# Optimization experiments

Hardware: AMD Instinct MI355X
Metric: run time of the kernel (lower is better)

Reference implementation:

```python
import jax, jax.numpy as jnp
import numpy as np

V, D, L = 256, 512, 12
B, S = 8, 8192
EPS = 1e-5


def layernorm(x, g, b):
    mu = jnp.mean(x, axis=-1, keepdims=True)
    var = jnp.var(x, axis=-1, keepdims=True)
    return (x - mu) * jax.lax.rsqrt(var + EPS) * g + b


def log_g(x):
    # log of g(x) = x+0.5 if x>=0 else sigmoid(x)
    return jnp.where(x >= 0, jnp.log(jax.nn.relu(x) + 0.5), -jax.nn.softplus(-x))


def heinsen_scan_log(log_coeffs, log_values):
    # h_t = a_t * h_{t-1} + b_t in log-space, parallel over seq (axis=1)
    a_star = jnp.cumsum(log_coeffs, axis=1)
    log_h0_plus_b = jax.lax.cumlogsumexp(log_values - a_star, axis=1)
    return jnp.exp(a_star + log_h0_plus_b)


def min_gru(x, W):
    hg = x @ W                      # [B,S,2D]
    hidden, gate = hg[..., :D], hg[..., D:]
    log_coeffs = -jax.nn.softplus(gate)      # log(1 - z)
    log_z = -jax.nn.softplus(-gate)          # log z
    log_values = log_z + log_g(hidden)
    return heinsen_scan_log(log_coeffs, log_values)


def setup_inputs() -> dict:
    key = jax.random.key(0)
    k0, k1, k2 = jax.random.split(key, 3)
    tokens = jax.random.randint(k0, (B, S), 0, V)
    emb = jax.random.normal(k1, (V, D), dtype=jnp.float32) * 0.02
    # xavier uniform for Linear(D, 2D): fan_in=D, fan_out=2D
    lim = float(np.sqrt(6.0 / (D + 2 * D)))
    W = jax.random.uniform(k2, (L, D, 2 * D), minval=-lim, maxval=lim, dtype=jnp.float32)
    return {
        "tokens": tokens,
        "emb": emb,
        "ln_g": jnp.ones((L, D), jnp.float32),
        "ln_b": jnp.zeros((L, D), jnp.float32),
        "W": W,
        "norm_g": jnp.ones((D,), jnp.float32),
        "norm_b": jnp.zeros((D,), jnp.float32),
    }


def reference(tokens, emb, ln_g, ln_b, W, norm_g, norm_b):
    x = emb[tokens]                 # [B,S,D]
    for i in range(L):
        h = layernorm(x, ln_g[i], ln_b[i])
        x = x + min_gru(h, W[i])
    x = layernorm(x, norm_g, norm_b)
    logits = x @ emb.T              # tied lm_head, [B,S,V]
    return logits
```

## Files before the change

### kernel.cpp

```cpp
#include <hip/hip_runtime.h>
#include <stdint.h>

#define D 512
#define VOCAB 256
#define NLAYER 12
#define BB 8
#define SS 8192
#define CH 128
#define SL 64

typedef __bf16 bf16x8 __attribute__((ext_vector_type(8)));
typedef float f32x4 __attribute__((ext_vector_type(4)));
typedef _Float16 half2_t __attribute__((ext_vector_type(2)));

__device__ __forceinline__ unsigned short f2bf(float f) {
  union { float f; uint32_t u; } c; c.f = f;
  uint32_t u = c.u;
  u += 0x7FFFu + ((u >> 16) & 1u);
  return (unsigned short)(u >> 16);
}

__device__ __forceinline__ float rcpf_(float x) { return __builtin_amdgcn_rcpf(x); }

__device__ __forceinline__ uint32_t pack_fv(float f, float v) {
  union { half2_t h; uint32_t u; } c;
  c.h.x = (_Float16)f;
  c.h.y = (_Float16)v;
  return c.u;
}

__device__ __forceinline__ void unpack_fv(uint32_t u, float& f, float& v) {
  union { uint32_t u; half2_t h; } c; c.u = u;
  f = (float)c.h.x;
  v = (float)c.h.y;
}

__device__ __forceinline__ void gl_lds16(const unsigned short* g, unsigned short* l) {
  __builtin_amdgcn_global_load_lds((const __attribute__((address_space(1))) void*)(const void*)g,
                                   (__attribute__((address_space(3))) void*)(void*)l, 16, 0, 0);
}

__global__ __launch_bounds__(256) void k_gather(const int* __restrict__ toks,
                                                const float* __restrict__ emb,
                                                const float* __restrict__ g,
                                                const float* __restrict__ b,
                                                float* __restrict__ x,
                                                unsigned short* __restrict__ o) {
  int T = blockIdx.x * 256 + threadIdx.x;
  int row = T >> 6, lane = T & 63;
  int tok = toks[row] & (VOCAB - 1);
  const float4* s = (const float4*)(emb + (size_t)tok * D) + lane * 2;
  float4 v0 = s[0], v1 = s[1];
  float4* d = (float4*)(x + (size_t)row * D) + lane * 2;
  d[0] = v0;
  d[1] = v1;
  float sm = v0.x + v0.y + v0.z + v0.w + v1.x + v1.y + v1.z + v1.w;
  float ss = v0.x * v0.x + v0.y * v0.y + v0.z * v0.z + v0.w * v0.w +
             v1.x * v1.x + v1.y * v1.y + v1.z * v1.z + v1.w * v1.w;
  for (int m = 32; m; m >>= 1) {
    sm += __shfl_xor(sm, m, 64);
    ss += __shfl_xor(ss, m, 64);
  }
  float mu = sm * (1.0f / 512.0f);
  float var = ss * (1.0f / 512.0f) - mu * mu;
  float rstd = rsqrtf(var + 1e-5f);
  const float4* gp = (const float4*)g + lane * 2;
  const float4* bp = (const float4*)b + lane * 2;
  float4 g0 = gp[0], g1 = gp[1], b0 = bp[0], b1 = bp[1];
  uint32_t w0 = (uint32_t)f2bf((v0.x - mu) * rstd * g0.x + b0.x) |
                ((uint32_t)f2bf((v0.y - mu) * rstd * g0.y + b0.y) << 16);
  uint32_t w1 = (uint32_t)f2bf((v0.z - mu) * rstd * g0.z + b0.z) |
                ((uint32_t)f2bf((v0.w - mu) * rstd * g0.w + b0.w) << 16);
  uint32_t w2 = (uint32_t)f2bf((v1.x - mu) * rstd * g1.x + b1.x) |
                ((uint32_t)f2bf((v1.y - mu) * rstd * g1.y + b1.y) << 16);
  uint32_t w3 = (uint32_t)f2bf((v1.z - mu) * rstd * g1.z + b1.z) |
                ((uint32_t)f2bf((v1.w - mu) * rstd * g1.w + b1.w) << 16);
  uint4 r; r.x = w0; r.y = w1; r.z = w2; r.w = w3;
  ((uint4*)(o + (size_t)row * D))[lane] = r;
}

__global__ __launch_bounds__(256) void k_convW(const float* __restrict__ W,
                                               unsigned short* __restrict__ Wt) {
  __shared__ float tile[32][33];
  int bid = blockIdx.x;
  int l = bid >> 9;
  int rem = bid & 511;
  int kt = rem >> 5, nt = rem & 31;
  int k0 = kt * 32, n0 = nt * 32;
  int tx = threadIdx.x & 31, ty = threadIdx.x >> 5;
  const float* Wl = W + (size_t)l * D * 2 * D;
  for (int i = 0; i < 4; i++) {
    int k = k0 + ty + 8 * i;
    tile[ty + 8 * i][tx] = Wl[(size_t)k * 1024 + n0 + tx];
  }
  __syncthreads();
  unsigned short* Wtl = Wt + (size_t)l * 1024 * D;
  for (int i = 0; i < 4; i++) {
    int n = n0 + ty + 8 * i;
    Wtl[(size_t)n * D + k0 + tx] = f2bf(tile[tx][ty + 8 * i]);
  }
}

__global__ __launch_bounds__(256) void k_fragW(const unsigned short* __restrict__ Wt,
                                               unsigned short* __restrict__ WtF) {
  int t = blockIdx.x * 256 + threadIdx.x;
  int lane = t & 63;
  int tile = t >> 6;
  int l = tile >> 10;
  int rem = tile & 1023;
  int n16 = rem >> 4, kt = rem & 15;
  const unsigned short* src = Wt + (size_t)l * 1024 * 512 +
                              (size_t)(n16 * 16 + (lane & 15)) * 512 + kt * 32 + (lane >> 4) * 8;
  *(uint4*)(WtF + (size_t)l * 524288 + ((size_t)rem * 64 + lane) * 8) = *(const uint4*)src;
}

__global__ __launch_bounds__(256) void k_convEmb(const float* __restrict__ e,
                                                 unsigned short* __restrict__ o) {
  int t = blockIdx.x * 256 + threadIdx.x;
  const float4* s = (const float4*)e + (size_t)t * 2;
  float4 a = s[0], b = s[1];
  uint32_t w0 = (uint32_t)f2bf(a.x) | ((uint32_t)f2bf(a.y) << 16);
  uint32_t w1 = (uint32_t)f2bf(a.z) | ((uint32_t)f2bf(a.w) << 16);
  uint32_t w2 = (uint32_t)f2bf(b.x) | ((uint32_t)f2bf(b.y) << 16);
  uint32_t w3 = (uint32_t)f2bf(b.z) | ((uint32_t)f2bf(b.w) << 16);
  uint4 r; r.x = w0; r.y = w1; r.z = w2; r.w = w3;
  ((uint4*)o)[t] = r;
}

__global__ __launch_bounds__(256, 2) void k_gemm_act(const unsigned short* __restrict__ A,
                                                     const unsigned short* __restrict__ Bt,
                                                     uint32_t* __restrict__ fv,
                                                     float* __restrict__ P,
                                                     float* __restrict__ Q) {
  __shared__ __align__(16) unsigned short As[64 * 512];
  const int tid = threadIdx.x;
  const int lane = tid & 63;
  const int wave = tid >> 6;
  const int m0 = blockIdx.x * 64;
  const int qm = lane & 15;
  const int hi = lane >> 4;
  for (int j = 0; j < 16; j++) {
    int r = wave * 16 + j;
    int cg = (lane & ~7) | ((lane & 7) ^ (r & 7));
    gl_lds16(A + (size_t)(m0 + r) * 512 + cg * 8, As + r * 512);
  }
  __syncthreads();

  const int b_loc = m0 >> 13;
  const int c_chunk = (m0 & (SS - 1)) >> 6;
  const size_t pq0 = ((size_t)b_loc * CH + c_chunk) * 512;

  for (int np = 0; np < 2; np++) {
    const int c0 = np * 256 + wave * 64;
    const int n16h = (c0 >> 4);
    f32x4 ah[4][4] = {};
    f32x4 ag[4][4] = {};
    bf16x8 bh[2][4], bg[2][4];
    for (int j = 0; j < 4; j++) {
      bh[0][j] = *(const bf16x8*)(Bt + (((size_t)(n16h + j) * 16 + 0) * 64 + lane) * 8);
      bg[0][j] = *(const bf16x8*)(Bt + (((size_t)(n16h + j + 32) * 16 + 0) * 64 + lane) * 8);
    }
    for (int kt = 0; kt < 16; kt++) {
      const int cur = kt & 1;
      if (kt < 15) {
        const int nxt = cur ^ 1;
        for (int j = 0; j < 4; j++) {
          bh[nxt][j] = *(const bf16x8*)(Bt + (((size_t)(n16h + j) * 16 + kt + 1) * 64 + lane) * 8);
          bg[nxt][j] = *(const bf16x8*)(Bt + (((size_t)(n16h + j + 32) * 16 + kt + 1) * 64 + lane) * 8);
        }
      }
      bf16x8 af[4];
      for (int i = 0; i < 4; i++) {
        int row = i * 16 + qm;
        int cgd = kt * 4 + hi;
        int cl = (cgd & ~7) | ((cgd & 7) ^ (row & 7));
        af[i] = *(const bf16x8*)(&As[row * 512 + cl * 8]);
      }
      for (int i = 0; i < 4; i++)
        for (int j = 0; j < 4; j++) {
          ah[i][j] = __builtin_amdgcn_mfma_f32_16x16x32_bf16(af[i], bh[cur][j], ah[i][j], 0, 0, 0);
          ag[i][j] = __builtin_amdgcn_mfma_f32_16x16x32_bf16(af[i], bg[cur][j], ag[i][j], 0, 0, 0);
        }
    }
    const int rq = hi * 4;
    for (int j = 0; j < 4; j++) {
      float cp = 1.f, cq = 0.f;
      for (int i = 0; i < 4; i++) {
        float sp = 1.f, sq = 0.f;
        for (int r = 0; r < 4; r++) {
          float h = ah[i][j][r];
          float g = ag[i][j][r];
          float e = __expf(g);
          float f = rcpf_(1.0f + e);
          float sg = 1.0f - f;
          float gf = h >= 0.0f ? h + 0.5f : rcpf_(1.0f + __expf(-h));
          float v = sg * gf;
          int rowg = m0 + i * 16 + rq + r;
          fv[(size_t)rowg * 512 + c0 + j * 16 + qm] = pack_fv(f, v);
          sp *= f;
          sq = sq * f + v;
        }
        float op = __shfl_xor(sp, 16), oq = __shfl_xor(sq, 16);
        float tp = sp * op;
        float tq = (lane & 16) ? (oq * sp + sq) : (sq * op + oq);
        op = __shfl_xor(tp, 32); oq = __shfl_xor(tq, 32);
        sp = tp * op;
        sq = (lane & 32) ? (oq * tp + tq) : (tq * op + oq);
        cq = cq * sp + sq;
        cp = cp * sp;
      }
      if (hi == 0) {
        P[pq0 + c0 + j * 16 + qm] = cp;
        Q[pq0 + c0 + j * 16 + qm] = cq;
      }
    }
  }
}

__global__ __launch_bounds__(256) void k_gemm(const unsigned short* __restrict__ A,
                                              const unsigned short* __restrict__ Bt,
                                              float* __restrict__ C, int N, int MT) {
  __shared__ __align__(16) unsigned short As[128 * 64];
  __shared__ __align__(16) unsigned short Bs[128 * 64];
  const int tid = threadIdx.x;
  const int lane = tid & 63;
  const int wave = tid >> 6;
  const int bid = blockIdx.x;
  const int mt = bid % MT;
  const int nt = bid / MT;
  const int m0 = mt * 128, n0 = nt * 128;
  const int wr = (wave >> 1) * 64;
  const int wc = (wave & 1) * 64;
  const int lrow = lane >> 3;
  const int lcs = ((lane & 7) ^ lrow) * 8;
  const unsigned short* Ag = A + (size_t)(m0 + wave * 32 + lrow) * 512 + lcs;
  const unsigned short* Bg = Bt + (size_t)(n0 + wave * 32 + lrow) * 512 + lcs;
  unsigned short* Al = As + wave * 32 * 64;
  unsigned short* Bl = Bs + wave * 32 * 64;
  const int qm = lane & 15;
  const int hi = lane >> 4;
  f32x4 acc[4][4] = {};
  for (int k0 = 0; k0 < 512; k0 += 64) {
    for (int j = 0; j < 4; j++) gl_lds16(Ag + k0 + (size_t)j * 8 * 512, Al + j * 512);
    for (int j = 0; j < 4; j++) gl_lds16(Bg + k0 + (size_t)j * 8 * 512, Bl + j * 512);
    __syncthreads();
    for (int ks = 0; ks < 2; ks++) {
      const int sw = ((ks * 4 + hi) ^ (qm & 7)) * 8;
      bf16x8 af[4], bfr[4];
      for (int i = 0; i < 4; i++) {
        af[i] = *(const bf16x8*)(&As[(wr + i * 16 + qm) * 64 + sw]);
        bfr[i] = *(const bf16x8*)(&Bs[(wc + i * 16 + qm) * 64 + sw]);
      }
      for (int i = 0; i < 4; i++)
        for (int j = 0; j < 4; j++)
          acc[i][j] = __builtin_amdgcn_mfma_f32_16x16x32_bf16(af[i], bfr[j], acc[i][j], 0, 0, 0);
    }
    __syncthreads();
  }
  const int col = lane & 15;
  const int rq = (lane >> 4) * 4;
  for (int i = 0; i < 4; i++)
    for (int j = 0; j < 4; j++)
      for (int r = 0; r < 4; r++)
        C[(size_t)(m0 + wr + i * 16 + rq + r) * N + (n0 + wc + j * 16 + col)] = acc[i][j][r];
}

__global__ __launch_bounds__(512) void k_scan2(const float* __restrict__ P,
                                               const float* __restrict__ Q,
                                               float* __restrict__ Hs) {
  __shared__ float lp[8][64];
  __shared__ float lq[8][64];
  const int lane = threadIdx.x & 63;
  const int w = threadIdx.x >> 6;
  const int dg = blockIdx.x & 7;
  const int b = blockIdx.x >> 3;
  const int d = dg * 64 + lane;
  const int c0 = w * 16;
  const size_t base = (size_t)b * CH * 512 + d;
  float p = 1.f, q = 0.f;
  for (int c = c0; c < c0 + 16; c++) {
    size_t i = base + (size_t)c * 512;
    float Pc = P[i], Qc = Q[i];
    q = q * Pc + Qc;
    p = p * Pc;
  }
  lp[w][lane] = p;
  lq[w][lane] = q;
  __syncthreads();
  float qq = 0.f, pp = 1.f;
  for (int ww = 0; ww < w; ww++) {
    float a = lp[ww][lane], bq = lq[ww][lane];
    qq = qq * a + bq;
    pp = pp * a;
  }
  float h = qq;
  for (int c = c0; c < c0 + 16; c++) {
    size_t i = base + (size_t)c * 512;
    Hs[i] = h;
    h = P[i] * h + Q[i];
  }
  (void)pp;
}

__global__ __launch_bounds__(512) void k_scan3(const uint32_t* __restrict__ fv,
                                               const float* __restrict__ Hs,
                                               float* __restrict__ x,
                                               const float* __restrict__ g,
                                               const float* __restrict__ b,
                                               unsigned short* __restrict__ o) {
  const int d = threadIdx.x;
  const int bc = blockIdx.x;
  const int c = bc & (CH - 1);
  const int bb = bc >> 7;
  const size_t row0 = ((size_t)bb * SS + (size_t)c * SL);
  const uint32_t* base = fv + row0 * 512 + d;
  float* xb = x + row0 * 512 + d;
  float h = Hs[(size_t)bc * 512 + d];
  for (int s = 0; s < SL; s++) {
    float f, v;
    unpack_fv(base[(size_t)s * 512], f, v);
    h = f * h + v;
    xb[(size_t)s * 512] += h;
  }
  __syncthreads();

  const int wv = threadIdx.x >> 6, lane = threadIdx.x & 63;
  const float4* gp = (const float4*)g + lane * 2;
  const float4* bp = (const float4*)b + lane * 2;
  float4 g0 = gp[0], g1 = gp[1], b0 = bp[0], b1 = bp[1];
  const float* xr0 = x + row0 * 512;
  for (int rr = 0; rr < 8; rr++) {
    int r = wv * 8 + rr;
    const float4* xr = (const float4*)(xr0 + (size_t)r * 512) + lane * 2;
    float4 v0 = xr[0], v1 = xr[1];
    float sm = v0.x + v0.y + v0.z + v0.w + v1.x + v1.y + v1.z + v1.w;
    float ss = v0.x * v0.x + v0.y * v0.y + v0.z * v0.z + v0.w * v0.w +
               v1.x * v1.x + v1.y * v1.y + v1.z * v1.z + v1.w * v1.w;
    for (int m = 32; m; m >>= 1) {
      sm += __shfl_xor(sm, m, 64);
      ss += __shfl_xor(ss, m, 64);
    }
    float mu = sm * (1.0f / 512.0f);
    float var = ss * (1.0f / 512.0f) - mu * mu;
    float rstd = rsqrtf(var + 1e-5f);
    uint32_t w0 = (uint32_t)f2bf((v0.x - mu) * rstd * g0.x + b0.x) |
                  ((uint32_t)f2bf((v0.y - mu) * rstd * g0.y + b0.y) << 16);
    uint32_t w1 = (uint32_t)f2bf((v0.z - mu) * rstd * g0.z + b0.z) |
                  ((uint32_t)f2bf((v0.w - mu) * rstd * g0.w + b0.w) << 16);
    uint32_t w2 = (uint32_t)f2bf((v1.x - mu) * rstd * g1.x + b1.x) |
                  ((uint32_t)f2bf((v1.y - mu) * rstd * g1.y + b1.y) << 16);
    uint32_t w3 = (uint32_t)f2bf((v1.z - mu) * rstd * g1.z + b1.z) |
                  ((uint32_t)f2bf((v1.w - mu) * rstd * g1.w + b1.w) << 16);
    uint4 rr4; rr4.x = w0; rr4.y = w1; rr4.z = w2; rr4.w = w3;
    ((uint4*)(o + (row0 + r) * 512))[lane] = rr4;
  }
}

extern "C" void kernel_launch(void* const* d_in, const int* in_sizes, int n_in,
                              void* d_out, int out_size, void* d_ws, size_t ws_size,
                              hipStream_t stream) {
  const int* toks = (const int*)d_in[0];
  const float* emb = (const float*)d_in[1];
  const float* ln_g = (const float*)d_in[2];
  const float* ln_b = (const float*)d_in[3];
  const float* W = (const float*)d_in[4];
  const float* norm_g = (const float*)d_in[5];
  const float* norm_b = (const float*)d_in[6];
  float* out = (float*)d_out;

  const int gbs[4] = {8, 4, 2, 1};
  int GB = 1;
  for (int i = 0; i < 4; i++) {
    size_t MGv = (size_t)gbs[i] * SS;
    size_t need = MGv * 5120 + 2 * 12582912 + 262144 + (size_t)gbs[i] * 786432;
    if (need <= ws_size) { GB = gbs[i]; break; }
  }
  const int MG = GB * SS;
  const int MT128 = MG / 128;

  char* p = (char*)d_ws;
  float* x = (float*)p;                     p += (size_t)MG * 2048;
  uint32_t* fv = (uint32_t*)p;              p += (size_t)MG * 2048;
  unsigned short* hbf = (unsigned short*)p; p += (size_t)MG * 1024;
  unsigned short* Wtrow = (unsigned short*)p; p += 12582912;
  unsigned short* WtF = (unsigned short*)p;   p += 12582912;
  unsigned short* ebf = (unsigned short*)p;   p += 262144;
  float* P = (float*)p;                     p += (size_t)GB * 262144;
  float* Q = (float*)p;                     p += (size_t)GB * 262144;
  float* Hs = (float*)p;

  k_convW<<<NLAYER * 512, 256, 0, stream>>>(W, Wtrow);
  k_fragW<<<NLAYER * 1024 * 64 / 256, 256, 0, stream>>>(Wtrow, WtF);
  k_convEmb<<<64, 256, 0, stream>>>(emb, ebf);

  for (int g = 0; g < BB / GB; g++) {
    const int* tg = toks + (size_t)g * MG;
    float* outg = out + (size_t)g * MG * VOCAB;

    k_gather<<<MG / 4, 256, 0, stream>>>(tg, emb, ln_g, ln_b, x, hbf);
    for (int l = 0; l < NLAYER; l++) {
      k_gemm_act<<<MG / 64, 256, 0, stream>>>(hbf, WtF + (size_t)l * 524288, fv, P, Q);
      k_scan2<<<GB * 8, 512, 0, stream>>>(P, Q, Hs);
      const float* gn = (l < NLAYER - 1) ? (ln_g + (size_t)(l + 1) * D) : norm_g;
      const float* bn = (l < NLAYER - 1) ? (ln_b + (size_t)(l + 1) * D) : norm_b;
      k_scan3<<<GB * CH, 512, 0, stream>>>(fv, Hs, x, gn, bn, hbf);
    }
    k_gemm<<<2 * MT128, 256, 0, stream>>>(hbf, ebf, outg, VOCAB, MT128);
  }
}
```

Measured before the change: 2.894 ms.

## Fuse scan apply and layernorm into next layer's GEMM via chunk-local prefix scan

The GEMM epilogue now computes an intra-chunk inclusive prefix (cumulative F and local y) per row, so the final hidden state is just y + F*h0 with no sequential dependency. Applying that correction, the residual add and the next layer's layernorm are folded into the prologue of the following layer's GEMM kernel, which removes the separate per-layer scan3 launch and its sequential 64-step loop. Only one apply+LN kernel remains after the last layer. In exchange the GEMM kernel does extra global reads and writes of x and yF before its LDS load, waits on a full vmcnt drain, and the epilogue shuffle work grows.

```diff
diff --git a/kernel.cpp b/kernel.cpp
--- a/kernel.cpp
+++ b/kernel.cpp
@@ -127,11 +127,16 @@
   ((uint4*)o)[t] = r;
 }
 
-__global__ __launch_bounds__(256, 2) void k_gemm_act(const unsigned short* __restrict__ A,
+__global__ __launch_bounds__(256, 2) void k_gemm_act(float* __restrict__ X,
+                                                     uint32_t* __restrict__ yF,
+                                                     const float* __restrict__ Hs,
+                                                     const float* __restrict__ lng,
+                                                     const float* __restrict__ lnb,
+                                                     unsigned short* __restrict__ Ah,
                                                      const unsigned short* __restrict__ Bt,
-                                                     uint32_t* __restrict__ fv,
                                                      float* __restrict__ P,
-                                                     float* __restrict__ Q) {
+                                                     float* __restrict__ Q,
+                                                     int APPLY) {
   __shared__ __align__(16) unsigned short As[64 * 512];
   const int tid = threadIdx.x;
   const int lane = tid & 63;
@@ -139,16 +144,63 @@
   const int m0 = blockIdx.x * 64;
   const int qm = lane & 15;
   const int hi = lane >> 4;
+  const int b_loc = m0 >> 13;
+  const int c_chunk = (m0 & (SS - 1)) >> 6;
+  const size_t pq0 = ((size_t)b_loc * CH + c_chunk) * 512;
+
+  if (APPLY) {
+    const float4* hp = (const float4*)(Hs + pq0) + lane * 2;
+    float4 h0v = hp[0], h1v = hp[1];
+    const float4* gp = (const float4*)lng + lane * 2;
+    const float4* bp = (const float4*)lnb + lane * 2;
+    float4 gg0 = gp[0], gg1 = gp[1], bb0 = bp[0], bb1 = bp[1];
+    for (int j = 0; j < 16; j++) {
+      size_t row = (size_t)(m0 + wave * 16 + j);
+      float4* xp = (float4*)(X + row * 512) + lane * 2;
+      float4 x0 = xp[0], x1 = xp[1];
+      const uint4* yp = (const uint4*)(yF + row * 512) + lane * 2;
+      uint4 y0 = yp[0], y1 = yp[1];
+      float Ff, yy;
+      unpack_fv(y0.x, Ff, yy); x0.x += yy + Ff * h0v.x;
+      unpack_fv(y0.y, Ff, yy); x0.y += yy + Ff * h0v.y;
+      unpack_fv(y0.z, Ff, yy); x0.z += yy + Ff * h0v.z;
+      unpack_fv(y0.w, Ff, yy); x0.w += yy + Ff * h0v.w;
+      unpack_fv(y1.x, Ff, yy); x1.x += yy + Ff * h1v.x;
+      unpack_fv(y1.y, Ff, yy); x1.y += yy + Ff * h1v.y;
+      unpack_fv(y1.z, Ff, yy); x1.z += yy + Ff * h1v.z;
+      unpack_fv(y1.w, Ff, yy); x1.w += yy + Ff * h1v.w;
+      xp[0] = x0; xp[1] = x1;
+      float sm = x0.x + x0.y + x0.z + x0.w + x1.x + x1.y + x1.z + x1.w;
+      float ss = x0.x * x0.x + x0.y * x0.y + x0.z * x0.z + x0.w * x0.w +
+                 x1.x * x1.x + x1.y * x1.y + x1.z * x1.z + x1.w * x1.w;
+      for (int m = 32; m; m >>= 1) {
+        sm += __shfl_xor(sm, m, 64);
+        ss += __shfl_xor(ss, m, 64);
+      }
+      float mu = sm * (1.0f / 512.0f);
+      float var = ss * (1.0f / 512.0f) - mu * mu;
+      float rstd = rsqrtf(var + 1e-5f);
+      uint32_t w0 = (uint32_t)f2bf((x0.x - mu) * rstd * gg0.x + bb0.x) |
+                    ((uint32_t)f2bf((x0.y - mu) * rstd * gg0.y + bb0.y) << 16);
+      uint32_t w1 = (uint32_t)f2bf((x0.z - mu) * rstd * gg0.z + bb0.z) |
+                    ((uint32_t)f2bf((x0.w - mu) * rstd * gg0.w + bb0.w) << 16);
+      uint32_t w2 = (uint32_t)f2bf((x1.x - mu) * rstd * gg1.x + bb1.x) |
+                    ((uint32_t)f2bf((x1.y - mu) * rstd * gg1.y + bb1.y) << 16);
+      uint32_t w3 = (uint32_t)f2bf((x1.z - mu) * rstd * gg1.z + bb1.z) |
+                    ((uint32_t)f2bf((x1.w - mu) * rstd * gg1.w + bb1.w) << 16);
+      uint4 rr; rr.x = w0; rr.y = w1; rr.z = w2; rr.w = w3;
+      ((uint4*)(Ah + row * 512))[lane] = rr;
+    }
+    asm volatile("s_waitcnt vmcnt(0)" ::: "memory");
+    __builtin_amdgcn_sched_barrier(0);
+  }
+
   for (int j = 0; j < 16; j++) {
     int r = wave * 16 + j;
     int cg = (lane & ~7) | ((lane & 7) ^ (r & 7));
-    gl_lds16(A + (size_t)(m0 + r) * 512 + cg * 8, As + r * 512);
+    gl_lds16(Ah + (size_t)(m0 + r) * 512 + cg * 8, As + r * 512);
   }
   __syncthreads();
-
-  const int b_loc = m0 >> 13;
-  const int c_chunk = (m0 & (SS - 1)) >> 6;
-  const size_t pq0 = ((size_t)b_loc * CH + c_chunk) * 512;
 
   for (int np = 0; np < 2; np++) {
     const int c0 = np * 256 + wave * 64;
@@ -184,9 +236,11 @@
     }
     const int rq = hi * 4;
     for (int j = 0; j < 4; j++) {
-      float cp = 1.f, cq = 0.f;
+      float Bp = 1.f, Bq = 0.f;
       for (int i = 0; i < 4; i++) {
+        float fr[4], vr[4];
         float sp = 1.f, sq = 0.f;
+#pragma unroll
         for (int r = 0; r < 4; r++) {
           float h = ah[i][j][r];
           float g = ag[i][j][r];
@@ -195,23 +249,33 @@
           float sg = 1.0f - f;
           float gf = h >= 0.0f ? h + 0.5f : rcpf_(1.0f + __expf(-h));
           float v = sg * gf;
+          fr[r] = f; vr[r] = v;
+          sq = sq * f + v;
+          sp *= f;
+        }
+        float Ip = sp, Iq = sq;
+        float tp = __shfl_up(Ip, 16, 64), tq = __shfl_up(Iq, 16, 64);
+        if (hi >= 1) { Iq = tq * Ip + Iq; Ip = tp * Ip; }
+        tp = __shfl_up(Ip, 32, 64); tq = __shfl_up(Iq, 32, 64);
+        if (hi >= 2) { Iq = tq * Ip + Iq; Ip = tp * Ip; }
+        float Ep = __shfl_up(Ip, 16, 64), Eq = __shfl_up(Iq, 16, 64);
+        if (hi == 0) { Ep = 1.f; Eq = 0.f; }
+        float Tp = __shfl(Ip, 48 + qm, 64), Tq = __shfl(Iq, 48 + qm, 64);
+        float yv = Bq * Ep + Eq;
+        float Fv = Bp * Ep;
+#pragma unroll
+        for (int r = 0; r < 4; r++) {
+          yv = fr[r] * yv + vr[r];
+          Fv = Fv * fr[r];
           int rowg = m0 + i * 16 + rq + r;
-          fv[(size_t)rowg * 512 + c0 + j * 16 + qm] = pack_fv(f, v);
-          sp *= f;
-          sq = sq * f + v;
+          yF[(size_t)rowg * 512 + c0 + j * 16 + qm] = pack_fv(Fv, yv);
         }
-        float op = __shfl_xor(sp, 16), oq = __shfl_xor(sq, 16);
-        float tp = sp * op;
-        float tq = (lane & 16) ? (oq * sp + sq) : (sq * op + oq);
-        op = __shfl_xor(tp, 32); oq = __shfl_xor(tq, 32);
-        sp = tp * op;
-        sq = (lane & 32) ? (oq * tp + tq) : (tq * op + oq);
-        cq = cq * sp + sq;
-        cp = cp * sp;
+        Bq = Bq * Tp + Tq;
+        Bp = Bp * Tp;
       }
       if (hi == 0) {
-        P[pq0 + c0 + j * 16 + qm] = cp;
-        Q[pq0 + c0 + j * 16 + qm] = cq;
+        P[pq0 + c0 + j * 16 + qm] = Bp;
+        Q[pq0 + c0 + j * 16 + qm] = Bq;
       }
     }
   }
@@ -287,11 +351,10 @@
   lp[w][lane] = p;
   lq[w][lane] = q;
   __syncthreads();
-  float qq = 0.f, pp = 1.f;
+  float qq = 0.f;
   for (int ww = 0; ww < w; ww++) {
     float a = lp[ww][lane], bq = lq[ww][lane];
     qq = qq * a + bq;
-    pp = pp * a;
   }
   float h = qq;
   for (int c = c0; c < c0 + 16; c++) {
@@ -299,28 +362,26 @@
     Hs[i] = h;
     h = P[i] * h + Q[i];
   }
-  (void)pp;
-}
-
-__global__ __launch_bounds__(512) void k_scan3(const uint32_t* __restrict__ fv,
-                                               const float* __restrict__ Hs,
-                                               float* __restrict__ x,
-                                               const float* __restrict__ g,
-                                               const float* __restrict__ b,
-                                               unsigned short* __restrict__ o) {
+}
+
+__global__ __launch_bounds__(512) void k_apply_ln(const uint32_t* __restrict__ yF,
+                                                  const float* __restrict__ Hs,
+                                                  float* __restrict__ x,
+                                                  const float* __restrict__ g,
+                                                  const float* __restrict__ b,
+                                                  unsigned short* __restrict__ o) {
   const int d = threadIdx.x;
   const int bc = blockIdx.x;
   const int c = bc & (CH - 1);
   const int bb = bc >> 7;
   const size_t row0 = ((size_t)bb * SS + (size_t)c * SL);
-  const uint32_t* base = fv + row0 * 512 + d;
+  const uint32_t* base = yF + row0 * 512 + d;
   float* xb = x + row0 * 512 + d;
   float h = Hs[(size_t)bc * 512 + d];
   for (int s = 0; s < SL; s++) {
-    float f, v;
-    unpack_fv(base[(size_t)s * 512], f, v);
-    h = f * h + v;
-    xb[(size_t)s * 512] += h;
+    float F, y;
+    unpack_fv(base[(size_t)s * 512], F, y);
+    xb[(size_t)s * 512] += y + F * h;
   }
   __syncthreads();
 
@@ -380,7 +441,7 @@
 
   char* p = (char*)d_ws;
   float* x = (float*)p;                     p += (size_t)MG * 2048;
-  uint32_t* fv = (uint32_t*)p;              p += (size_t)MG * 2048;
+  uint32_t* yF = (uint32_t*)p;              p += (size_t)MG * 2048;
   unsigned short* hbf = (unsigned short*)p; p += (size_t)MG * 1024;
   unsigned short* Wtrow = (unsigned short*)p; p += 12582912;
   unsigned short* WtF = (unsigned short*)p;   p += 12582912;
@@ -399,12 +460,13 @@
 
     k_gather<<<MG / 4, 256, 0, stream>>>(tg, emb, ln_g, ln_b, x, hbf);
     for (int l = 0; l < NLAYER; l++) {
-      k_gemm_act<<<MG / 64, 256, 0, stream>>>(hbf, WtF + (size_t)l * 524288, fv, P, Q);
+      k_gemm_act<<<MG / 64, 256, 0, stream>>>(x, yF, Hs,
+                                              ln_g + (size_t)l * D, ln_b + (size_t)l * D,
+                                              hbf, WtF + (size_t)l * 524288, P, Q,
+                                              l > 0 ? 1 : 0);
       k_scan2<<<GB * 8, 512, 0, stream>>>(P, Q, Hs);
-      const float* gn = (l < NLAYER - 1) ? (ln_g + (size_t)(l + 1) * D) : norm_g;
-      const float* bn = (l < NLAYER - 1) ? (ln_b + (size_t)(l + 1) * D) : norm_b;
-      k_scan3<<<GB * CH, 512, 0, stream>>>(fv, Hs, x, gn, bn, hbf);
-    }
+    }
+    k_apply_ln<<<GB * CH, 512, 0, stream>>>(yF, Hs, x, norm_g, norm_b, hbf);
     k_gemm<<<2 * MT128, 256, 0, stream>>>(hbf, ebf, outg, VOCAB, MT128);
   }
 }
```

New measurement: 2.673 ms. -7.6%, faster.
